# Kernel optimization log

Hardware: AMD Instinct MI355X
Metric: run time of the kernel (lower is better)

Reference implementation:

```python
import jax, jax.numpy as jnp
import numpy as np

N_NODES = 131072
HIDDEN = 256
N_CLUSTERS = 64
NUM_GRAPHS = 64
MAX_NODES = 4096  # static pad length (>= max nodes per graph w.h.p.)


def setup_inputs() -> dict:
    key = jax.random.key(0)
    ks = jax.random.split(key, 12)
    d = HIDDEN
    xav = (6.0 / (2 * d)) ** 0.5  # xavier_uniform bound for square Linear / Q param
    x = jax.random.normal(ks[0], (N_NODES, d), dtype=jnp.float32)
    batch = jnp.sort(jax.random.randint(ks[1], (N_NODES,), 0, NUM_GRAPHS)).astype(jnp.int64)
    def lin(kw, kb):
        W = jax.random.uniform(kw, (d, d), dtype=jnp.float32, minval=-xav, maxval=xav)
        b = jax.random.uniform(kb, (d,), dtype=jnp.float32, minval=-d ** -0.5, maxval=d ** -0.5)
        return W, b
    Qp = jax.random.uniform(ks[2], (1, N_CLUSTERS, d), dtype=jnp.float32, minval=-xav, maxval=xav)
    WQ_w, WQ_b = lin(ks[3], ks[4])
    WK_w, WK_b = lin(ks[5], ks[6])
    WV_w, WV_b = lin(ks[7], ks[8])
    WO_w, WO_b = lin(ks[9], ks[10])
    return {"x": x, "batch": batch, "Qp": Qp,
            "WQ_w": WQ_w, "WQ_b": WQ_b, "WK_w": WK_w, "WK_b": WK_b,
            "WV_w": WV_w, "WV_b": WV_b, "WO_w": WO_w, "WO_b": WO_b}


def _dense_pos(batch):
    # position of each node within its graph (batch is sorted)
    ones = jnp.ones_like(batch, dtype=jnp.int32)
    counts = jax.ops.segment_sum(ones, batch, num_segments=NUM_GRAPHS)
    starts = jnp.cumsum(counts) - counts
    pos = jnp.arange(batch.shape[0], dtype=jnp.int32) - starts[batch]
    return pos


def reference(x, batch, Qp, WQ_w, WQ_b, WK_w, WK_b, WV_w, WV_b, WO_w, WO_b):
    d = x.shape[-1]
    pos = _dense_pos(batch)
    K = x @ WK_w.T + WK_b
    V = x @ WV_w.T + WV_b
    # to_dense_batch: scatter into [B, MAX_NODES, d] (out-of-range dropped)
    Kd = jnp.zeros((NUM_GRAPHS, MAX_NODES, d), x.dtype).at[batch, pos].set(K, mode='drop')
    Vd = jnp.zeros((NUM_GRAPHS, MAX_NODES, d), x.dtype).at[batch, pos].set(V, mode='drop')
    mask = jnp.zeros((NUM_GRAPHS, MAX_NODES), bool).at[batch, pos].set(True, mode='drop')
    attn_mask = (~mask).astype(x.dtype)[:, None, :] * (-1e9)  # [B,1,L]
    Q = jnp.broadcast_to(Qp, (NUM_GRAPHS, N_CLUSTERS, d)) @ WQ_w.T + WQ_b  # [B,C,d]
    A = jnp.einsum('bcd,bld->bcl', Q, Kd) / (d ** 0.5) + attn_mask
    A = jax.nn.softmax(A, axis=-2)  # inverted softmax: over cluster (query) axis
    out = Q + jnp.einsum('bcl,bld->bcd', A, Vd)
    out = jax.nn.relu(out @ WO_w.T + WO_b)  # residual=False branch
    return out, jnp.argmax(A, axis=-2), mask
```

## Files before the change

### kernel.cpp

```cpp
#include <hip/hip_runtime.h>

#define N_NODES 131072
#define MAXL 4096
#define NP 8

typedef __attribute__((ext_vector_type(8))) short bf16x8;
typedef __attribute__((ext_vector_type(4))) float f32x4;

#define OFF_QW     0u
#define OFF_QO     16384u
#define OFF_WF     32768u
#define OFF_QB     98304u
#define OFF_BVO    98368u
#define OFF_STARTS 98624u
#define OFF_ASUM   98752u
#define OFF_Q      102848u
#define OFF_WQT    119232u
#define OFF_WOT    184768u
#define OFF_GP     250304u

__device__ __forceinline__ unsigned short f2bf(float f) {
  union { float f; unsigned int u; } v; v.f = f;
  unsigned int u = v.u + 0x7FFFu + ((v.u >> 16) & 1u);
  return (unsigned short)(u >> 16);
}

__device__ __forceinline__ float xor1_add(float v) {
  int r = __builtin_amdgcn_update_dpp(0, __float_as_int(v), 0xB1, 0xF, 0xF, true);
  return v + __int_as_float(r);
}
__device__ __forceinline__ float xor2_add(float v) {
  int r = __builtin_amdgcn_update_dpp(0, __float_as_int(v), 0x4E, 0xF, 0xF, true);
  return v + __int_as_float(r);
}
__device__ __forceinline__ float xor4_add(float v) {
  int r = __builtin_amdgcn_ds_swizzle(__float_as_int(v), 0x101F);
  return v + __int_as_float(r);
}
__device__ __forceinline__ float kq_sum(float v) { return xor4_add(xor2_add(xor1_add(v))); }


__global__ __launch_bounds__(256) void k_tr(const float* __restrict__ WQ_w,
    const float* __restrict__ WO_w, float* __restrict__ WQT, float* __restrict__ WOT)
{
  __shared__ float tile[32][33];
  const float* src = blockIdx.z ? WO_w : WQ_w;
  float* dst = blockIdx.z ? WOT : WQT;
  const int bx = blockIdx.x * 32, by = blockIdx.y * 32;
  const int tx = threadIdx.x & 31, ty = threadIdx.x >> 5;
  #pragma unroll
  for (int i = 0; i < 4; ++i)
    tile[ty + 8 * i][tx] = src[(size_t)(by + ty + 8 * i) * 256 + bx + tx];
  __syncthreads();
  #pragma unroll
  for (int i = 0; i < 4; ++i)
    dst[(size_t)(bx + ty + 8 * i) * 256 + by + tx] = tile[tx][ty + 8 * i];
}

__global__ __launch_bounds__(256) void k_q(const float* __restrict__ Qp,
    const float* __restrict__ WQT, const float* __restrict__ WQ_b,
    float* __restrict__ Q)
{
  const int c = blockIdx.x, d = threadIdx.x;
  float acc = WQ_b[d];
  for (int k = 0; k < 256; ++k)
    acc += Qp[c * 256 + k] * WQT[k * 256 + d];
  Q[c * 256 + d] = acc;
}

__global__ __launch_bounds__(256) void k_fold(const float* __restrict__ Q,
    const float* __restrict__ WK_w, const float* __restrict__ WK_b,
    const float* __restrict__ WOT,
    float* __restrict__ QW, float* __restrict__ QO, float* __restrict__ qb)
{
  __shared__ float Qrow[256];
  const int c = blockIdx.x, d = threadIdx.x;
  Qrow[d] = Q[c * 256 + d];
  __syncthreads();
  double aqw = 0.0;
  float aqo = 0.f;
  for (int j = 0; j < 256; ++j) {
    float qcj = Qrow[j];
    aqw += (double)qcj * (double)WK_w[j * 256 + d];
    aqo += qcj * WOT[j * 256 + d];
  }
  QW[c * 256 + d] = (float)(aqw * 0.0625);
  QO[c * 256 + d] = aqo;
  if (d == 0) {
    double s = 0.0;
    for (int j = 0; j < 256; ++j) s += (double)Qrow[j] * (double)WK_b[j];
    qb[c] = (float)(s * 0.0625);
  }
}

__global__ __launch_bounds__(256) void k_wf(const float* __restrict__ WO_w,
    const float* __restrict__ WV_w, const float* __restrict__ WV_b,
    float* __restrict__ Wf, float* __restrict__ bvo)
{
  const int i = blockIdx.x, d = threadIdx.x;
  float acc = 0.f;
  for (int j = 0; j < 256; ++j)
    acc += WO_w[i * 256 + j] * WV_w[j * 256 + d];
  Wf[i * 256 + d] = acc;
  if (d == 0) {
    float s = 0.f;
    for (int j = 0; j < 256; ++j) s += WV_b[j] * WO_w[i * 256 + j];
    bvo[i] = s;
  }
}

__global__ void k_starts(const int* __restrict__ batch, int* __restrict__ starts)
{
  int t = threadIdx.x;
  if (t > 64) return;
  if (t == 0) { starts[0] = 0; return; }
  if (t == 64) { starts[64] = N_NODES; return; }
  int lo = 0, hi = N_NODES;
  while (lo < hi) {
    int mid = (lo + hi) >> 1;
    if (batch[mid] < t) lo = mid + 1; else hi = mid;
  }
  starts[t] = lo;
}


__global__ __launch_bounds__(256, 2) void k_fused(
    const float* __restrict__ x, const int* __restrict__ starts,
    const float* __restrict__ qw, const float* __restrict__ qbv,
    float* __restrict__ Gp, float* __restrict__ asum,
    float* __restrict__ out_arg, float* __restrict__ out_msk)
{
  __shared__ float xs[32][256];
  __shared__ float ss[32][68];
  __shared__ float stats_m[32], stats_i[32];
  __shared__ __align__(16) unsigned short As[64][40];
  __shared__ __align__(16) unsigned short XsT[256][40];

  const int t = threadIdx.x;
  const int p = blockIdx.x, b = blockIdx.y;
  const int s0 = starts[b], s1 = starts[b + 1];
  const int w = t >> 6, lane = t & 63;
  const int cp = lane >> 3, kq = lane & 7;
  const int c0 = w * 16 + cp, c1 = c0 + 8;

  const float qb0 = qbv[c0], qb1 = qbv[c1];
  const float* qg0 = qw + (size_t)c0 * 256 + kq * 16;
  const float* qg1 = qw + (size_t)c1 * 256 + kq * 16;

  f32x4 gacc[16];
  #pragma unroll
  for (int i = 0; i < 16; ++i) gacc[i] = (f32x4){0.f, 0.f, 0.f, 0.f};
  float asv0 = 0.f, asv1 = 0.f;

  const int stcol = (lane * 4) ^ (4 * ((lane >> 3) & 7));
  const int dsz   = t ^ (4 * ((t >> 5) & 7));

  #pragma unroll 1
  for (int base = s0 + p * 32; base < s1; base += NP * 32) {
    #pragma unroll
    for (int i = 0; i < 8; ++i) {
      int r = w * 8 + i;
      int gr = base + r; if (gr >= s1) gr = s1 - 1;
      float4 v = *(const float4*)&x[(size_t)gr * 256 + lane * 4];
      *(float4*)&xs[r][stcol] = v;
    }
    __syncthreads();
    #pragma unroll
    for (int g = 0; g < 8; ++g) {
      ushort4 pk;
      pk.x = f2bf(xs[g * 4 + 0][dsz]);
      pk.y = f2bf(xs[g * 4 + 1][dsz]);
      pk.z = f2bf(xs[g * 4 + 2][dsz]);
      pk.w = f2bf(xs[g * 4 + 3][dsz]);
      *(ushort4*)&XsT[t][g * 4] = pk;
    }
    #pragma unroll 1
    for (int h = 0; h < 4; ++h) {
      float a0[8], a1[8];
      #pragma unroll
      for (int n = 0; n < 8; ++n) { a0[n] = 0.f; a1[n] = 0.f; }
      const float* xb = &xs[h * 8][0];
      #pragma unroll 1
      for (int h2 = 0; h2 < 2; ++h2) {
        float4 qA0 = *(const float4*)&qg0[h2 * 128 + 0];
        float4 qA1 = *(const float4*)&qg0[h2 * 128 + 4];
        float4 qA2 = *(const float4*)&qg0[h2 * 128 + 8];
        float4 qA3 = *(const float4*)&qg0[h2 * 128 + 12];
        float4 qB0 = *(const float4*)&qg1[h2 * 128 + 0];
        float4 qB1 = *(const float4*)&qg1[h2 * 128 + 4];
        float4 qB2 = *(const float4*)&qg1[h2 * 128 + 8];
        float4 qB3 = *(const float4*)&qg1[h2 * 128 + 12];
        #pragma unroll
        for (int k4 = 0; k4 < 4; ++k4) {
          const int colb = h2 * 128 + kq * 16 + k4 * 4;
          const int col = colb ^ (4 * ((colb >> 5) & 7));
          const float4 qa = (k4 == 0) ? qA0 : (k4 == 1) ? qA1 : (k4 == 2) ? qA2 : qA3;
          const float4 qc = (k4 == 0) ? qB0 : (k4 == 1) ? qB1 : (k4 == 2) ? qB2 : qB3;
          #pragma unroll
          for (int n = 0; n < 8; ++n) {
            float4 xv = *(const float4*)&xb[n * 256 + col];
            a0[n] = fmaf(qa.w, xv.w, fmaf(qa.z, xv.z, fmaf(qa.y, xv.y, fmaf(qa.x, xv.x, a0[n]))));
            a1[n] = fmaf(qc.w, xv.w, fmaf(qc.z, xv.z, fmaf(qc.y, xv.y, fmaf(qc.x, xv.x, a1[n]))));
          }
        }
      }
      #pragma unroll
      for (int n = 0; n < 8; ++n) {
        float s0v = kq_sum(a0[n]);
        float s1v = kq_sum(a1[n]);
        if (kq == n) {
          ss[h * 8 + n][c0] = s0v + qb0;
          ss[h * 8 + n][c1] = s1v + qb1;
        }
      }
    }
    __syncthreads();
    {
      const int nn = t >> 3, oct = t & 7;
      float v8[8];
      #pragma unroll
      for (int u = 0; u < 8; ++u) v8[u] = ss[nn][oct * 8 + u];
      float m = v8[0]; int am = oct * 8;
      #pragma unroll
      for (int u = 1; u < 8; ++u)
        if (v8[u] > m) { m = v8[u]; am = oct * 8 + u; }
      #pragma unroll
      for (int d = 1; d < 8; d <<= 1) {
        float mo = __shfl_xor(m, d);
        int ao = __shfl_xor(am, d);
        if (mo > m || (mo == m && ao < am)) { m = mo; am = ao; }
      }
      float s = 0.f;
      #pragma unroll
      for (int u = 0; u < 8; ++u) s += __expf(v8[u] - m);
      #pragma unroll
      for (int d = 1; d < 8; d <<= 1) s += __shfl_xor(s, d);
      if (oct == 0) {
        stats_m[nn] = m;
        stats_i[nn] = 1.f / s;
        int n = base + nn;
        if (n < s1) {
          int pos = n - s0;
          out_arg[(size_t)b * MAXL + pos] = (float)am;
          out_msk[(size_t)b * MAXL + pos] = 1.0f;
        }
      }
    }
    __syncthreads();
    {
      unsigned short pb0[4], pb1[4];
      #pragma unroll
      for (int i = 0; i < 4; ++i) {
        int nn = 4 * kq + i;
        bool valid = (base + nn) < s1;
        float m = stats_m[nn], inv = stats_i[nn];
        float av0 = valid ? __expf(ss[nn][c0] - m) * inv : 0.f;
        float av1 = valid ? __expf(ss[nn][c1] - m) * inv : 0.f;
        asv0 += av0; asv1 += av1;
        pb0[i] = f2bf(av0);
        pb1[i] = f2bf(av1);
      }
      *(ushort4*)&As[c0][4 * kq] = *(const ushort4*)pb0;
      *(ushort4*)&As[c1][4 * kq] = *(const ushort4*)pb1;
    }
    __syncthreads();
    {
      const int q = lane >> 4, mm = lane & 15;
      bf16x8 afrag = *(const bf16x8*)&As[16 * w + mm][q * 8];
      #pragma unroll
      for (int dt = 0; dt < 16; ++dt) {
        bf16x8 bfrag = *(const bf16x8*)&XsT[16 * dt + mm][q * 8];
        gacc[dt] = __builtin_amdgcn_mfma_f32_16x16x32_bf16(afrag, bfrag, gacc[dt], 0, 0, 0);
      }
    }
    __syncthreads();
  }

  {
    float* g = Gp + ((size_t)p * 64 + b) * 16384;
    const int q = lane >> 4, mm = lane & 15;
    #pragma unroll
    for (int dt = 0; dt < 16; ++dt)
      #pragma unroll
      for (int r = 0; r < 4; ++r)
        g[(size_t)(16 * w + q * 4 + r) * 256 + 16 * dt + mm] = gacc[dt][r];
  }
  asv0 = kq_sum(asv0);
  asv1 = kq_sum(asv1);
  if (kq == 0) {
    atomicAdd(&asum[b * 64 + c0], asv0);
    atomicAdd(&asum[b * 64 + c1], asv1);
  }
}


__global__ __launch_bounds__(256) void k_final(const float* __restrict__ Gp,
    int npart, const float* __restrict__ Wf, const float* __restrict__ qo,
    const float* __restrict__ asum, const float* __restrict__ bvo,
    const float* __restrict__ WO_b, float* __restrict__ out)
{
  __shared__ float gs[64 * 68];
  __shared__ float wfs[64 * 68];
  const int t = threadIdx.x;
  const int b = blockIdx.x >> 2;
  const int is = (blockIdx.x & 3) * 64;
  const int tx = t & 15, ty = t >> 4;
  const int sr = t >> 4, sq = t & 15;

  float acc[4][4];
  #pragma unroll
  for (int j = 0; j < 4; ++j)
    #pragma unroll
    for (int u = 0; u < 4; ++u) acc[j][u] = 0.f;

  for (int kc = 0; kc < 4; ++kc) {
    const int k0 = kc * 64;
    #pragma unroll
    for (int u = 0; u < 4; ++u) {
      int row = sr + 16 * u;
      float4 g = make_float4(0.f, 0.f, 0.f, 0.f);
      for (int p = 0; p < npart; ++p) {
        float4 gv = *(const float4*)&Gp[((size_t)p * 64 + b) * 16384
                                        + row * 256 + k0 + sq * 4];
        g.x += gv.x; g.y += gv.y; g.z += gv.z; g.w += gv.w;
      }
      *(float4*)&gs[row * 68 + sq * 4] = g;
      *(float4*)&wfs[row * 68 + sq * 4] =
          *(const float4*)&Wf[(size_t)(is + row) * 256 + k0 + sq * 4];
    }
    __syncthreads();
    #pragma unroll
    for (int k4 = 0; k4 < 16; ++k4) {
      float4 gr[4], wr[4];
      #pragma unroll
      for (int j = 0; j < 4; ++j) gr[j] = *(const float4*)&gs[(ty + 16 * j) * 68 + k4 * 4];
      #pragma unroll
      for (int u = 0; u < 4; ++u) wr[u] = *(const float4*)&wfs[(tx + 16 * u) * 68 + k4 * 4];
      #pragma unroll
      for (int j = 0; j < 4; ++j)
        #pragma unroll
        for (int u = 0; u < 4; ++u)
          acc[j][u] += gr[j].x * wr[u].x + gr[j].y * wr[u].y
                     + gr[j].z * wr[u].z + gr[j].w * wr[u].w;
    }
    __syncthreads();
  }

  #pragma unroll
  for (int j = 0; j < 4; ++j)
    #pragma unroll
    for (int u = 0; u < 4; ++u) {
      int cc = ty + 16 * j, i = is + tx + 16 * u;
      float v = acc[j][u] + qo[cc * 256 + i] + asum[b * 64 + cc] * bvo[i] + WO_b[i];
      out[(size_t)b * 16384 + cc * 256 + i] = fmaxf(v, 0.f);
    }
}


extern "C" void kernel_launch(void* const* d_in, const int* in_sizes, int n_in,
                              void* d_out, int out_size, void* d_ws, size_t ws_size,
                              hipStream_t stream) {
  const float* x    = (const float*)d_in[0];
  const int*   batch= (const int*)d_in[1];
  const float* Qp   = (const float*)d_in[2];
  const float* WQ_w = (const float*)d_in[3];
  const float* WQ_b = (const float*)d_in[4];
  const float* WK_w = (const float*)d_in[5];
  const float* WK_b = (const float*)d_in[6];
  const float* WV_w = (const float*)d_in[7];
  const float* WV_b = (const float*)d_in[8];
  const float* WO_w = (const float*)d_in[9];
  const float* WO_b = (const float*)d_in[10];

  float* ws   = (float*)d_ws;
  float* QW   = ws + OFF_QW;
  float* QO   = ws + OFF_QO;
  float* Wf   = ws + OFF_WF;
  float* qb   = ws + OFF_QB;
  float* bvo  = ws + OFF_BVO;
  int*   starts = (int*)(ws + OFF_STARTS);
  float* asum = ws + OFF_ASUM;
  float* Q    = ws + OFF_Q;
  float* WQT  = ws + OFF_WQT;
  float* WOT  = ws + OFF_WOT;
  float* Gp   = ws + OFF_GP;

  float* out     = (float*)d_out;
  float* out_arg = out + 64 * 64 * 256;
  float* out_msk = out_arg + 64 * MAXL;

  hipMemsetAsync(asum, 0, 64 * 64 * sizeof(float), stream);
  hipMemsetAsync(out_arg, 0, (size_t)2 * 64 * MAXL * sizeof(float), stream);

  k_tr<<<dim3(8, 8, 2), 256, 0, stream>>>(WQ_w, WO_w, WQT, WOT);
  k_wf<<<256, 256, 0, stream>>>(WO_w, WV_w, WV_b, Wf, bvo);
  k_starts<<<1, 128, 0, stream>>>(batch, starts);
  k_q<<<64, 256, 0, stream>>>(Qp, WQT, WQ_b, Q);
  k_fold<<<64, 256, 0, stream>>>(Q, WK_w, WK_b, WOT, QW, QO, qb);

  k_fused<<<dim3(NP, 64), 256, 0, stream>>>(x, starts, QW, qb, Gp, asum,
                                            out_arg, out_msk);
  k_final<<<64 * 4, 256, 0, stream>>>(Gp, NP, Wf, QO, asum, bvo, WO_b, out);
}
```

Before: 450.2 us.

## Split reduction dims across more threads in prep kernels and double fused block width

The small precompute kernels (k_q, k_fold, k_wf) now use 1024 threads per block. The 256-long reduction is split into four 64-long slices, then combined through shared memory. The serial qb dot product becomes a tree reduction. The main fused kernel moves to 512-thread blocks: two wave halves share the score rows and the MFMA output columns, with half the accumulators per wave, to improve latency hiding. The cost is more synchronisation and some idle threads in the softmax stats phase.

Result: no change. 450.7 us (+0.1%).

```diff
diff --git a/kernel.cpp b/kernel.cpp
--- a/kernel.cpp
+++ b/kernel.cpp
@@ -57,55 +57,82 @@
     dst[(size_t)(bx + ty + 8 * i) * 256 + by + tx] = tile[tx][ty + 8 * i];
 }
 
-__global__ __launch_bounds__(256) void k_q(const float* __restrict__ Qp,
+__global__ __launch_bounds__(1024) void k_q(const float* __restrict__ Qp,
     const float* __restrict__ WQT, const float* __restrict__ WQ_b,
     float* __restrict__ Q)
 {
-  const int c = blockIdx.x, d = threadIdx.x;
-  float acc = WQ_b[d];
-  for (int k = 0; k < 256; ++k)
+  __shared__ float red[4][256];
+  const int c = blockIdx.x, t = threadIdx.x;
+  const int d = t & 255, kk = t >> 8;
+  float acc = 0.f;
+  #pragma unroll 4
+  for (int k = kk * 64; k < kk * 64 + 64; ++k)
     acc += Qp[c * 256 + k] * WQT[k * 256 + d];
-  Q[c * 256 + d] = acc;
-}
-
-__global__ __launch_bounds__(256) void k_fold(const float* __restrict__ Q,
+  red[kk][d] = acc;
+  __syncthreads();
+  if (kk == 0)
+    Q[c * 256 + d] = red[0][d] + red[1][d] + red[2][d] + red[3][d] + WQ_b[d];
+}
+
+__global__ __launch_bounds__(1024) void k_fold(const float* __restrict__ Q,
     const float* __restrict__ WK_w, const float* __restrict__ WK_b,
     const float* __restrict__ WOT,
     float* __restrict__ QW, float* __restrict__ QO, float* __restrict__ qb)
 {
   __shared__ float Qrow[256];
-  const int c = blockIdx.x, d = threadIdx.x;
-  Qrow[d] = Q[c * 256 + d];
+  __shared__ double redw[4][256];
+  __shared__ float redo[4][256];
+  const int c = blockIdx.x, t = threadIdx.x;
+  const int d = t & 255, kk = t >> 8;
+  if (t < 256) Qrow[t] = Q[c * 256 + t];
   __syncthreads();
   double aqw = 0.0;
   float aqo = 0.f;
-  for (int j = 0; j < 256; ++j) {
+  #pragma unroll 4
+  for (int j = kk * 64; j < kk * 64 + 64; ++j) {
     float qcj = Qrow[j];
     aqw += (double)qcj * (double)WK_w[j * 256 + d];
     aqo += qcj * WOT[j * 256 + d];
   }
-  QW[c * 256 + d] = (float)(aqw * 0.0625);
-  QO[c * 256 + d] = aqo;
-  if (d == 0) {
-    double s = 0.0;
-    for (int j = 0; j < 256; ++j) s += (double)Qrow[j] * (double)WK_b[j];
-    qb[c] = (float)(s * 0.0625);
-  }
-}
-
-__global__ __launch_bounds__(256) void k_wf(const float* __restrict__ WO_w,
+  redw[kk][d] = aqw;
+  redo[kk][d] = aqo;
+  __syncthreads();
+  if (kk == 0) {
+    QW[c * 256 + d] = (float)((redw[0][d] + redw[1][d] + redw[2][d] + redw[3][d]) * 0.0625);
+    QO[c * 256 + d] = redo[0][d] + redo[1][d] + redo[2][d] + redo[3][d];
+  }
+  __syncthreads();
+  if (t < 256) redw[0][t] = (double)Qrow[t] * (double)WK_b[t];
+  __syncthreads();
+  for (int sft = 128; sft >= 1; sft >>= 1) {
+    if (t < sft) redw[0][t] += redw[0][t + sft];
+    __syncthreads();
+  }
+  if (t == 0) qb[c] = (float)(redw[0][0] * 0.0625);
+}
+
+__global__ __launch_bounds__(1024) void k_wf(const float* __restrict__ WO_w,
     const float* __restrict__ WV_w, const float* __restrict__ WV_b,
     float* __restrict__ Wf, float* __restrict__ bvo)
 {
-  const int i = blockIdx.x, d = threadIdx.x;
+  __shared__ float red[4][256];
+  __shared__ float redb[4];
+  const int i = blockIdx.x, t = threadIdx.x;
+  const int d = t & 255, kk = t >> 8;
   float acc = 0.f;
-  for (int j = 0; j < 256; ++j)
+  #pragma unroll 4
+  for (int j = kk * 64; j < kk * 64 + 64; ++j)
     acc += WO_w[i * 256 + j] * WV_w[j * 256 + d];
-  Wf[i * 256 + d] = acc;
+  red[kk][d] = acc;
   if (d == 0) {
     float s = 0.f;
-    for (int j = 0; j < 256; ++j) s += WV_b[j] * WO_w[i * 256 + j];
-    bvo[i] = s;
+    for (int j = kk * 64; j < kk * 64 + 64; ++j) s += WV_b[j] * WO_w[i * 256 + j];
+    redb[kk] = s;
+  }
+  __syncthreads();
+  if (kk == 0) {
+    Wf[i * 256 + d] = red[0][d] + red[1][d] + red[2][d] + red[3][d];
+    if (d == 0) bvo[i] = redb[0] + redb[1] + redb[2] + redb[3];
   }
 }
 
@@ -124,7 +151,7 @@
 }
 
 
-__global__ __launch_bounds__(256, 2) void k_fused(
+__global__ __launch_bounds__(512, 4) void k_fused(
     const float* __restrict__ x, const int* __restrict__ starts,
     const float* __restrict__ qw, const float* __restrict__ qbv,
     float* __restrict__ Gp, float* __restrict__ asum,
@@ -140,67 +167,88 @@
   const int p = blockIdx.x, b = blockIdx.y;
   const int s0 = starts[b], s1 = starts[b + 1];
   const int w = t >> 6, lane = t & 63;
+  const int wg = w & 3, wh = w >> 2;
   const int cp = lane >> 3, kq = lane & 7;
-  const int c0 = w * 16 + cp, c1 = c0 + 8;
+  const int c0 = wg * 16 + cp, c1 = c0 + 8;
 
   const float qb0 = qbv[c0], qb1 = qbv[c1];
   const float* qg0 = qw + (size_t)c0 * 256 + kq * 16;
   const float* qg1 = qw + (size_t)c1 * 256 + kq * 16;
 
-  f32x4 gacc[16];
+  f32x4 gacc[8];
   #pragma unroll
-  for (int i = 0; i < 16; ++i) gacc[i] = (f32x4){0.f, 0.f, 0.f, 0.f};
+  for (int i = 0; i < 8; ++i) gacc[i] = (f32x4){0.f, 0.f, 0.f, 0.f};
   float asv0 = 0.f, asv1 = 0.f;
 
   const int stcol = (lane * 4) ^ (4 * ((lane >> 3) & 7));
-  const int dsz   = t ^ (4 * ((t >> 5) & 7));
+  const int dX = t & 255, hX = t >> 8;
+  const int dsz = dX ^ (4 * ((dX >> 5) & 7));
 
   #pragma unroll 1
   for (int base = s0 + p * 32; base < s1; base += NP * 32) {
     #pragma unroll
-    for (int i = 0; i < 8; ++i) {
-      int r = w * 8 + i;
+    for (int i = 0; i < 4; ++i) {
+      int r = w * 4 + i;
       int gr = base + r; if (gr >= s1) gr = s1 - 1;
       float4 v = *(const float4*)&x[(size_t)gr * 256 + lane * 4];
       *(float4*)&xs[r][stcol] = v;
     }
     __syncthreads();
     #pragma unroll
-    for (int g = 0; g < 8; ++g) {
+    for (int g = 0; g < 4; ++g) {
+      const int r0 = hX * 16 + g * 4;
       ushort4 pk;
-      pk.x = f2bf(xs[g * 4 + 0][dsz]);
-      pk.y = f2bf(xs[g * 4 + 1][dsz]);
-      pk.z = f2bf(xs[g * 4 + 2][dsz]);
-      pk.w = f2bf(xs[g * 4 + 3][dsz]);
-      *(ushort4*)&XsT[t][g * 4] = pk;
+      pk.x = f2bf(xs[r0 + 0][dsz]);
+      pk.y = f2bf(xs[r0 + 1][dsz]);
+      pk.z = f2bf(xs[r0 + 2][dsz]);
+      pk.w = f2bf(xs[r0 + 3][dsz]);
+      *(ushort4*)&XsT[dX][r0] = pk;
     }
     #pragma unroll 1
-    for (int h = 0; h < 4; ++h) {
+    for (int hh = 0; hh < 2; ++hh) {
+      const int h = wh * 2 + hh;
       float a0[8], a1[8];
       #pragma unroll
       for (int n = 0; n < 8; ++n) { a0[n] = 0.f; a1[n] = 0.f; }
       const float* xb = &xs[h * 8][0];
       #pragma unroll 1
       for (int h2 = 0; h2 < 2; ++h2) {
-        float4 qA0 = *(const float4*)&qg0[h2 * 128 + 0];
-        float4 qA1 = *(const float4*)&qg0[h2 * 128 + 4];
-        float4 qA2 = *(const float4*)&qg0[h2 * 128 + 8];
-        float4 qA3 = *(const float4*)&qg0[h2 * 128 + 12];
-        float4 qB0 = *(const float4*)&qg1[h2 * 128 + 0];
-        float4 qB1 = *(const float4*)&qg1[h2 * 128 + 4];
-        float4 qB2 = *(const float4*)&qg1[h2 * 128 + 8];
-        float4 qB3 = *(const float4*)&qg1[h2 * 128 + 12];
-        #pragma unroll
-        for (int k4 = 0; k4 < 4; ++k4) {
-          const int colb = h2 * 128 + kq * 16 + k4 * 4;
-          const int col = colb ^ (4 * ((colb >> 5) & 7));
-          const float4 qa = (k4 == 0) ? qA0 : (k4 == 1) ? qA1 : (k4 == 2) ? qA2 : qA3;
-          const float4 qc = (k4 == 0) ? qB0 : (k4 == 1) ? qB1 : (k4 == 2) ? qB2 : qB3;
+        {
+          float4 qa0 = *(const float4*)&qg0[h2 * 128 + 0];
+          float4 qa1 = *(const float4*)&qg0[h2 * 128 + 4];
+          float4 qc0 = *(const float4*)&qg1[h2 * 128 + 0];
+          float4 qc1 = *(const float4*)&qg1[h2 * 128 + 4];
           #pragma unroll
-          for (int n = 0; n < 8; ++n) {
-            float4 xv = *(const float4*)&xb[n * 256 + col];
-            a0[n] = fmaf(qa.w, xv.w, fmaf(qa.z, xv.z, fmaf(qa.y, xv.y, fmaf(qa.x, xv.x, a0[n]))));
-            a1[n] = fmaf(qc.w, xv.w, fmaf(qc.z, xv.z, fmaf(qc.y, xv.y, fmaf(qc.x, xv.x, a1[n]))));
+          for (int k4 = 0; k4 < 2; ++k4) {
+            const int colb = h2 * 128 + kq * 16 + k4 * 4;
+            const int col = colb ^ (4 * ((colb >> 5) & 7));
+            const float4 qa = k4 ? qa1 : qa0;
+            const float4 qc = k4 ? qc1 : qc0;
+            #pragma unroll
+            for (int n = 0; n < 8; ++n) {
+              float4 xv = *(const float4*)&xb[n * 256 + col];
+              a0[n] = fmaf(qa.w, xv.w, fmaf(qa.z, xv.z, fmaf(qa.y, xv.y, fmaf(qa.x, xv.x, a0[n]))));
+              a1[n] = fmaf(qc.w, xv.w, fmaf(qc.z, xv.z, fmaf(qc.y, xv.y, fmaf(qc.x, xv.x, a1[n]))));
+            }
+          }
+        }
+        {
+          float4 qa2 = *(const float4*)&qg0[h2 * 128 + 8];
+          float4 qa3 = *(const float4*)&qg0[h2 * 128 + 12];
+          float4 qc2 = *(const float4*)&qg1[h2 * 128 + 8];
+          float4 qc3 = *(const float4*)&qg1[h2 * 128 + 12];
+          #pragma unroll
+          for (int k4 = 2; k4 < 4; ++k4) {
+            const int colb = h2 * 128 + kq * 16 + k4 * 4;
+            const int col = colb ^ (4 * ((colb >> 5) & 7));
+            const float4 qa = (k4 == 2) ? qa2 : qa3;
+            const float4 qc = (k4 == 2) ? qc2 : qc3;
+            #pragma unroll
+            for (int n = 0; n < 8; ++n) {
+              float4 xv = *(const float4*)&xb[n * 256 + col];
+              a0[n] = fmaf(qa.w, xv.w, fmaf(qa.z, xv.z, fmaf(qa.y, xv.y, fmaf(qa.x, xv.x, a0[n]))));
+              a1[n] = fmaf(qc.w, xv.w, fmaf(qc.z, xv.z, fmaf(qc.y, xv.y, fmaf(qc.x, xv.x, a1[n]))));
+            }
           }
         }
       }
@@ -215,7 +263,7 @@
       }
     }
     __syncthreads();
-    {
+    if (t < 256) {
       const int nn = t >> 3, oct = t & 7;
       float v8[8];
       #pragma unroll
@@ -248,10 +296,10 @@
     }
     __syncthreads();
     {
-      unsigned short pb0[4], pb1[4];
-      #pragma unroll
-      for (int i = 0; i < 4; ++i) {
-        int nn = 4 * kq + i;
+      unsigned short pb0[2], pb1[2];
+      #pragma unroll
+      for (int i = 0; i < 2; ++i) {
+        int nn = 4 * kq + 2 * wh + i;
         bool valid = (base + nn) < s1;
         float m = stats_m[nn], inv = stats_i[nn];
         float av0 = valid ? __expf(ss[nn][c0] - m) * inv : 0.f;
@@ -260,17 +308,18 @@
         pb0[i] = f2bf(av0);
         pb1[i] = f2bf(av1);
       }
-      *(ushort4*)&As[c0][4 * kq] = *(const ushort4*)pb0;
-      *(ushort4*)&As[c1][4 * kq] = *(const ushort4*)pb1;
+      *(ushort2*)&As[c0][4 * kq + 2 * wh] = *(const ushort2*)pb0;
+      *(ushort2*)&As[c1][4 * kq + 2 * wh] = *(const ushort2*)pb1;
     }
     __syncthreads();
     {
       const int q = lane >> 4, mm = lane & 15;
-      bf16x8 afrag = *(const bf16x8*)&As[16 * w + mm][q * 8];
-      #pragma unroll
-      for (int dt = 0; dt < 16; ++dt) {
+      bf16x8 afrag = *(const bf16x8*)&As[16 * wg + mm][q * 8];
+      #pragma unroll
+      for (int dt2 = 0; dt2 < 8; ++dt2) {
+        const int dt = wh * 8 + dt2;
         bf16x8 bfrag = *(const bf16x8*)&XsT[16 * dt + mm][q * 8];
-        gacc[dt] = __builtin_amdgcn_mfma_f32_16x16x32_bf16(afrag, bfrag, gacc[dt], 0, 0, 0);
+        gacc[dt2] = __builtin_amdgcn_mfma_f32_16x16x32_bf16(afrag, bfrag, gacc[dt2], 0, 0, 0);
       }
     }
     __syncthreads();
@@ -280,10 +329,12 @@
     float* g = Gp + ((size_t)p * 64 + b) * 16384;
     const int q = lane >> 4, mm = lane & 15;
     #pragma unroll
-    for (int dt = 0; dt < 16; ++dt)
+    for (int dt2 = 0; dt2 < 8; ++dt2) {
+      const int dt = wh * 8 + dt2;
       #pragma unroll
       for (int r = 0; r < 4; ++r)
-        g[(size_t)(16 * w + q * 4 + r) * 256 + 16 * dt + mm] = gacc[dt][r];
+        g[(size_t)(16 * wg + q * 4 + r) * 256 + 16 * dt + mm] = gacc[dt2][r];
+    }
   }
   asv0 = kq_sum(asv0);
   asv1 = kq_sum(asv1);
@@ -393,12 +444,12 @@
   hipMemsetAsync(out_arg, 0, (size_t)2 * 64 * MAXL * sizeof(float), stream);
 
   k_tr<<<dim3(8, 8, 2), 256, 0, stream>>>(WQ_w, WO_w, WQT, WOT);
-  k_wf<<<256, 256, 0, stream>>>(WO_w, WV_w, WV_b, Wf, bvo);
+  k_wf<<<256, 1024, 0, stream>>>(WO_w, WV_w, WV_b, Wf, bvo);
   k_starts<<<1, 128, 0, stream>>>(batch, starts);
-  k_q<<<64, 256, 0, stream>>>(Qp, WQT, WQ_b, Q);
-  k_fold<<<64, 256, 0, stream>>>(Q, WK_w, WK_b, WOT, QW, QO, qb);
-
-  k_fused<<<dim3(NP, 64), 256, 0, stream>>>(x, starts, QW, qb, Gp, asum,
+  k_q<<<64, 1024, 0, stream>>>(Qp, WQT, WQ_b, Q);
+  k_fold<<<64, 1024, 0, stream>>>(Q, WK_w, WK_b, WOT, QW, QO, qb);
+
+  k_fused<<<dim3(NP, 64), 512, 0, stream>>>(x, starts, QW, qb, Gp, asum,
                                             out_arg, out_msk);
   k_final<<<64 * 4, 256, 0, stream>>>(Gp, NP, Wf, QO, asum, bvo, WO_b, out);
 }
```
